# Kernel tuning notes

Measured on AMD Instinct MI355X. Metric: run time of the kernel, lower is better.

The kernel has to match this reference:

```python
import jax, jax.numpy as jnp
import numpy as np

B, S, E, H = 2, 2048, 1024, 16
D = E // H  # head_dim = 64


def setup_inputs() -> dict:
    key = jax.random.key(0)
    ks = jax.random.split(key, 8)
    s = 0.02
    return {
        "queries": jax.random.normal(ks[0], (B, S, E), jnp.float32),
        "keys": jax.random.normal(ks[1], (B, S, E), jnp.float32),
        "values": jax.random.normal(ks[2], (B, S, E), jnp.float32),
        "mask": jnp.ones((B, 1, 1, S), jnp.int32),
        "Wq": jax.random.normal(ks[3], (E, E), jnp.float32) * s,
        "bq": jnp.zeros((E,), jnp.float32),
        "Wk": jax.random.normal(ks[4], (E, E), jnp.float32) * s,
        "bk": jnp.zeros((E,), jnp.float32),
        "Wv": jax.random.normal(ks[5], (E, E), jnp.float32) * s,
        "bv": jnp.zeros((E,), jnp.float32),
        "Wo": jax.random.normal(ks[6], (E, E), jnp.float32) * s,
        "bo": jnp.zeros((E,), jnp.float32),
    }


def reference(queries, keys, values, mask, Wq, bq, Wk, bk, Wv, bv, Wo, bo):
    # NOTE: faithful to source, W_v is applied to the `keys` input; `values` is unused.
    q = queries @ Wq.T + bq            # [B,S,E]
    k = keys @ Wk.T + bk               # [B,S,E]
    v = keys @ Wv.T + bv               # [B,S,E]
    q = q.reshape(B, S, H, D)
    k = k.reshape(B, S, H, D)
    v = v.reshape(B, S, H, D)
    scale = 1.0 / jnp.sqrt(jnp.asarray(D, q.dtype))
    scores = jnp.einsum("nqhd,nkhd->nhqk", q, k)   # [B,H,S,S] full score matrix
    scores = jnp.where(mask == 0, jnp.asarray(-1e20, scores.dtype), scores)
    attn = jax.nn.softmax(scores * scale, axis=-1)
    out = jnp.einsum("nhqk,nkhd->nqhd", attn, v).reshape(B, S, E)
    return out @ Wo.T + bo
```

## Files before the change

kernel.cpp:

```cpp
#include <hip/hip_runtime.h>
#include <hip/hip_bf16.h>
#include <stdint.h>

#define NB 2
#define NS 2048
#define NE 1024
#define NH 16
#define ND 64
#define NT 32

typedef __attribute__((ext_vector_type(4))) float f32x4;
typedef __attribute__((ext_vector_type(16))) float f32x16;
typedef __attribute__((ext_vector_type(8))) short s16x8;
typedef __attribute__((ext_vector_type(4))) unsigned short u16x4;
typedef __attribute__((ext_vector_type(2))) unsigned int uint2v;

__device__ __forceinline__ unsigned short f2bf(float f) {
  union { float f; unsigned int i; } u; u.f = f;
  unsigned int r = u.i + 0x7FFFu + ((u.i >> 16) & 1u);
  return (unsigned short)(r >> 16);
}

__device__ __forceinline__ unsigned cvtpk_bf16(float lo, float hi) {
  unsigned r;
  asm("v_cvt_pk_bf16_f32 %0, %1, %2" : "=v"(r) : "v"(lo), "v"(hi));
  return r;
}

__device__ __forceinline__ void gload_lds16(const void* g, void* l) {
  __builtin_amdgcn_global_load_lds(
      (const __attribute__((address_space(1))) uint32_t*)g,
      (__attribute__((address_space(3))) uint32_t*)l, 16, 0, 0);
}

__device__ __forceinline__ f32x4 mfma16(s16x8 a, s16x8 b, f32x4 c) {
  return __builtin_amdgcn_mfma_f32_16x16x32_bf16(a, b, c, 0, 0, 0);
}
__device__ __forceinline__ f32x16 mfma32(s16x8 a, s16x8 b, f32x16 c) {
  return __builtin_amdgcn_mfma_f32_32x32x16_bf16(a, b, c, 0, 0, 0);
}

__global__ void conv_x2(const float* __restrict__ a, const float* __restrict__ b,
                        unsigned short* __restrict__ da, unsigned short* __restrict__ db,
                        int n4) {
  const float* s = blockIdx.y ? b : a;
  unsigned short* d = blockIdx.y ? db : da;
  int i = blockIdx.x * blockDim.x + threadIdx.x;
  int stride = gridDim.x * blockDim.x;
  for (; i < n4; i += stride) {
    float4 v = ((const float4*)s)[i];
    u16x4 o;
    o.x = f2bf(v.x); o.y = f2bf(v.y); o.z = f2bf(v.z); o.w = f2bf(v.w);
    ((u16x4*)d)[i] = o;
  }
}

__global__ void conv_w4(const float* __restrict__ s0, const float* __restrict__ s1,
                        const float* __restrict__ s2, const float* __restrict__ s3,
                        unsigned short* __restrict__ d0, unsigned short* __restrict__ d1,
                        unsigned short* __restrict__ d2, unsigned short* __restrict__ d3,
                        int n4) {
  const float* s; unsigned short* d;
  switch (blockIdx.y) {
    case 0: s = s0; d = d0; break;
    case 1: s = s1; d = d1; break;
    case 2: s = s2; d = d2; break;
    default: s = s3; d = d3; break;
  }
  int i = blockIdx.x * blockDim.x + threadIdx.x;
  int stride = gridDim.x * blockDim.x;
  for (; i < n4; i += stride) {
    float4 v = ((const float4*)s)[i];
    u16x4 o;
    o.x = f2bf(v.x); o.y = f2bf(v.y); o.z = f2bf(v.z); o.w = f2bf(v.w);
    ((u16x4*)d)[i] = o;
  }
}

__global__ void mask_pack(const int* __restrict__ mask, unsigned long long* __restrict__ bm) {
  int w = blockIdx.x;
  int lane = threadIdx.x;
  int mk = mask[w * 64 + lane];
  unsigned long long bal = __ballot(mk != 0);
  if (lane == 0) bm[w] = bal;
}

__global__ __launch_bounds__(256, 3) void gemm_qkv(
    const unsigned short* __restrict__ Aq, const unsigned short* __restrict__ Akv,
    const unsigned short* __restrict__ Wqp, const unsigned short* __restrict__ Wkp,
    const unsigned short* __restrict__ Wvp,
    const float* __restrict__ bqp, const float* __restrict__ bkp, const float* __restrict__ bvp,
    unsigned short* __restrict__ outq, unsigned short* __restrict__ outk,
    unsigned short* __restrict__ outvt) {
  constexpr int BM = 64, K = 1024;
  __shared__ char smem[2 * (BM * 128 + 16384)];
  const int t = threadIdx.x;
  const int lane = t & 63;
  const int wv = t >> 6;
  const int wr = wv >> 1, wc = wv & 1;
  const int x = blockIdx.x;
  const int bm = blockIdx.y * BM;
  const int lr = lane & 15, lg = lane >> 4;

  const unsigned short* A; const unsigned short* Wp; const float* bp;
  unsigned short* outp; int nloc, mode;
  float qsc;
  if (x < 8)       { A = Aq;  Wp = Wqp; bp = bqp; outp = outq;  nloc = x * 128;        mode = 0; qsc = 0.18033688f; }
  else if (x < 16) { A = Akv; Wp = Wkp; bp = bkp; outp = outk;  nloc = (x - 8) * 128;  mode = 0; qsc = 1.0f; }
  else             { A = Akv; Wp = Wvp; bp = bvp; outp = outvt; nloc = (x - 16) * 128; mode = 1; qsc = 1.0f; }

  f32x4 acc[2][4] = {};

  auto stage = [&](int buf, int k0) {
    char* As = smem + buf * (BM * 128 + 16384);
    char* Bs = As + BM * 128;
#pragma unroll
    for (int r = 0; r < 2; ++r) {
      int lin = r * 256 + t;
      int row = lin >> 3;
      int scb = ((lin & 7) << 4) ^ ((row & 7) << 4);
      gload_lds16((const char*)(A + (size_t)(bm + row) * K + k0) + scb,
                  As + (size_t)(r * 256 + (t & ~63)) * 16);
    }
#pragma unroll
    for (int r = 0; r < 4; ++r) {
      int lin = r * 256 + t;
      int row = lin >> 3;
      int scb = ((lin & 7) << 4) ^ ((row & 7) << 4);
      gload_lds16((const char*)(Wp + (size_t)(nloc + row) * K + k0) + scb,
                  Bs + (size_t)(r * 256 + (t & ~63)) * 16);
    }
  };

  stage(0, 0);
  for (int t6 = 0; t6 < K / 64; ++t6) {
    const int cur = t6 & 1;
    if (t6 + 1 < K / 64) {
      stage(cur ^ 1, (t6 + 1) * 64);
      asm volatile("s_waitcnt vmcnt(6)" ::: "memory");
    } else {
      asm volatile("s_waitcnt vmcnt(0)" ::: "memory");
    }
    asm volatile("s_barrier" ::: "memory");

    const char* As = smem + cur * (BM * 128 + 16384);
    const char* Bs = As + BM * 128;
    s16x8 af[2][2], bfr[4][2];
#pragma unroll
    for (int mf = 0; mf < 2; ++mf)
#pragma unroll
      for (int kk = 0; kk < 2; ++kk) {
        int row = wr * 32 + mf * 16 + lr;
        int cb = (lg << 4) + (kk << 6);
        af[mf][kk] = *(const s16x8*)(As + row * 128 + (cb ^ ((row & 7) << 4)));
      }
#pragma unroll
    for (int nf = 0; nf < 4; ++nf)
#pragma unroll
      for (int kk = 0; kk < 2; ++kk) {
        int row = wc * 64 + nf * 16 + lr;
        int cb = (lg << 4) + (kk << 6);
        bfr[nf][kk] = *(const s16x8*)(Bs + row * 128 + (cb ^ ((row & 7) << 4)));
      }
#pragma unroll
    for (int mf = 0; mf < 2; ++mf)
#pragma unroll
      for (int nf = 0; nf < 4; ++nf)
#pragma unroll
        for (int kk = 0; kk < 2; ++kk)
          acc[mf][nf] = mfma16(af[mf][kk], bfr[nf][kk], acc[mf][nf]);

    asm volatile("s_waitcnt lgkmcnt(0)" ::: "memory");
    asm volatile("s_barrier" ::: "memory");
  }

#pragma unroll
  for (int mf = 0; mf < 2; ++mf)
#pragma unroll
    for (int nf = 0; nf < 4; ++nf) {
      int m0 = bm + wr * 32 + mf * 16 + (lg << 2);
      int nc = wc * 64 + nf * 16 + lr;
      float bv = bp[nloc + nc];
      if (mode == 0) {
#pragma unroll
        for (int r = 0; r < 4; ++r)
          outp[(size_t)(m0 + r) * 1024 + nloc + nc] = f2bf((acc[mf][nf][r] + bv) * qsc);
      } else {
        int b = m0 >> 11, s = m0 & 2047;
        u16x4 o;
        o.x = f2bf(acc[mf][nf][0] + bv);
        o.y = f2bf(acc[mf][nf][1] + bv);
        o.z = f2bf(acc[mf][nf][2] + bv);
        o.w = f2bf(acc[mf][nf][3] + bv);
        *(u16x4*)&outp[((size_t)b * NE + nloc + nc) * NS + s] = o;
      }
    }
}

__global__ __launch_bounds__(256, 3) void gemm_o(
    const unsigned short* __restrict__ A, const unsigned short* __restrict__ W,
    const float* __restrict__ bias, float* __restrict__ out) {
  constexpr int BM = 64, K = 1024;
  __shared__ char smem[2 * (BM * 128 + 16384)];
  const int t = threadIdx.x;
  const int lane = t & 63;
  const int wv = t >> 6;
  const int wr = wv >> 1, wc = wv & 1;
  const int bm = blockIdx.y * BM, bn = blockIdx.x * 128;
  const int lr = lane & 15, lg = lane >> 4;

  f32x4 acc[2][4] = {};

  auto stage = [&](int buf, int k0) {
    char* As = smem + buf * (BM * 128 + 16384);
    char* Bs = As + BM * 128;
#pragma unroll
    for (int r = 0; r < 2; ++r) {
      int lin = r * 256 + t;
      int row = lin >> 3;
      int scb = ((lin & 7) << 4) ^ ((row & 7) << 4);
      gload_lds16((const char*)(A + (size_t)(bm + row) * K + k0) + scb,
                  As + (size_t)(r * 256 + (t & ~63)) * 16);
    }
#pragma unroll
    for (int r = 0; r < 4; ++r) {
      int lin = r * 256 + t;
      int row = lin >> 3;
      int scb = ((lin & 7) << 4) ^ ((row & 7) << 4);
      gload_lds16((const char*)(W + (size_t)(bn + row) * K + k0) + scb,
                  Bs + (size_t)(r * 256 + (t & ~63)) * 16);
    }
  };

  stage(0, 0);
  for (int t6 = 0; t6 < K / 64; ++t6) {
    const int cur = t6 & 1;
    if (t6 + 1 < K / 64) {
      stage(cur ^ 1, (t6 + 1) * 64);
      asm volatile("s_waitcnt vmcnt(6)" ::: "memory");
    } else {
      asm volatile("s_waitcnt vmcnt(0)" ::: "memory");
    }
    asm volatile("s_barrier" ::: "memory");

    const char* As = smem + cur * (BM * 128 + 16384);
    const char* Bs = As + BM * 128;
    s16x8 af[2][2], bfr[4][2];
#pragma unroll
    for (int mf = 0; mf < 2; ++mf)
#pragma unroll
      for (int kk = 0; kk < 2; ++kk) {
        int row = wr * 32 + mf * 16 + lr;
        int cb = (lg << 4) + (kk << 6);
        af[mf][kk] = *(const s16x8*)(As + row * 128 + (cb ^ ((row & 7) << 4)));
      }
#pragma unroll
    for (int nf = 0; nf < 4; ++nf)
#pragma unroll
      for (int kk = 0; kk < 2; ++kk) {
        int row = wc * 64 + nf * 16 + lr;
        int cb = (lg << 4) + (kk << 6);
        bfr[nf][kk] = *(const s16x8*)(Bs + row * 128 + (cb ^ ((row & 7) << 4)));
      }
#pragma unroll
    for (int mf = 0; mf < 2; ++mf)
#pragma unroll
      for (int nf = 0; nf < 4; ++nf)
#pragma unroll
        for (int kk = 0; kk < 2; ++kk)
          acc[mf][nf] = mfma16(af[mf][kk], bfr[nf][kk], acc[mf][nf]);

    asm volatile("s_waitcnt lgkmcnt(0)" ::: "memory");
    asm volatile("s_barrier" ::: "memory");
  }

#pragma unroll
  for (int mf = 0; mf < 2; ++mf)
#pragma unroll
    for (int nf = 0; nf < 4; ++nf) {
      int m0 = bm + wr * 32 + mf * 16 + (lg << 2);
      int n = bn + wc * 64 + nf * 16 + lr;
      float bv = bias[n];
#pragma unroll
      for (int r = 0; r < 4; ++r)
        out[(size_t)(m0 + r) * 1024 + n] = acc[mf][nf][r] + bv;
    }
}

__global__ __launch_bounds__(256, 2) void attn_fwd(
    const unsigned short* __restrict__ qb, const unsigned short* __restrict__ kb,
    const unsigned short* __restrict__ vt, const unsigned long long* __restrict__ bmw,
    unsigned short* __restrict__ ob) {
  __shared__ char smem[65536];
  const int t = threadIdx.x, lane = t & 63, wv = t >> 6;
  const int l31 = lane & 31, hi = lane >> 5;
  const int sw = (l31 & 15) << 4;
  const int bh = blockIdx.y, b = bh >> 4, h = bh & 15;
  const int q = blockIdx.x * 128 + wv * 32 + l31;

  s16x8 qf[4];
#pragma unroll
  for (int ks = 0; ks < 4; ++ks)
    qf[ks] = *(const s16x8*)&qb[((size_t)(b * NS + q)) * NE + h * ND + ks * 16 + hi * 8];

  unsigned long long mword = bmw[(size_t)b * 32 + l31];
  unsigned mlo = (unsigned)mword, mhi = (unsigned)(mword >> 32);

  const char* kSrc[2]; const char* vSrc[2]; int ldsK[2], ldsV[2];
#pragma unroll
  for (int r = 0; r < 2; ++r) {
    int L = (r * 256 + t) * 16;
    int row = L >> 8;
    int offp = (L & 255) ^ ((row & 15) << 4);
    int rr = row + ((offp >> 7) << 5);
    int byo = offp & 127;
    kSrc[r] = (const char*)&kb[((size_t)(b * NS) + rr) * NE + h * ND] + byo;
    vSrc[r] = (const char*)&vt[((size_t)((b * NH + h) * ND) + rr) * NS] + byo;
    ldsK[r] = (r * 256 + (t & ~63)) * 16;
    ldsV[r] = 8192 + ldsK[r];
  }

  int off16[8];
#pragma unroll
  for (int j = 0; j < 8; ++j)
    off16[j] = l31 * 256 + ((j * 32 + hi * 16) ^ sw);

  auto stage = [&](int buf, int kt) {
    char* base = smem + buf * 16384;
#pragma unroll
    for (int r = 0; r < 2; ++r)
      gload_lds16(kSrc[r] + (size_t)kt * (NE * 2), base + ldsK[r]);
#pragma unroll
    for (int r = 0; r < 2; ++r)
      gload_lds16(vSrc[r] + (size_t)kt * 2, base + ldsV[r]);
  };

  f32x16 oacc[2] = {};
  f32x16 lacc = {};

  auto compute = [&](int tt, const char* Ks) {
    const char* Vs = Ks + 8192;

    f32x16 st0 = {}, st1 = {};
    __builtin_amdgcn_s_setprio(1);
#pragma unroll
    for (int ks = 0; ks < 4; ++ks) {
      s16x8 kf = *(const s16x8*)(Ks + off16[ks]);
      st0 = mfma32(kf, qf[ks], st0);
    }
#pragma unroll
    for (int ks = 0; ks < 4; ++ks) {
      s16x8 kf = *(const s16x8*)(Ks + off16[4 + ks]);
      st1 = mfma32(kf, qf[ks], st1);
    }
    __builtin_amdgcn_s_setprio(0);

#pragma unroll
    for (int r = 0; r < 16; ++r) st0[r] = __builtin_amdgcn_exp2f(st0[r] - 6.0f);
#pragma unroll
    for (int r = 0; r < 16; ++r) st1[r] = __builtin_amdgcn_exp2f(st1[r] - 6.0f);

    unsigned lo = (unsigned)__builtin_amdgcn_readlane((int)mlo, tt);
    unsigned hh = (unsigned)__builtin_amdgcn_readlane((int)mhi, tt);
    unsigned long long bal = ((unsigned long long)hh << 32) | lo;
    if (bal != ~0ull) {
#pragma unroll
      for (int r = 0; r < 16; ++r) {
        int key0 = (r & 3) + 8 * (r >> 2) + 4 * hi;
        if (!((bal >> key0) & 1)) st0[r] = 0.f;
        if (!((bal >> (key0 + 32)) & 1)) st1[r] = 0.f;
      }
    }

    lacc += st0;
    lacc += st1;

    s16x8 pf[4];
#pragma unroll
    for (int ks = 0; ks < 4; ++ks) {
      const int r0 = (ks & 1) * 8;
      unsigned wreg[4];
#pragma unroll
      for (int w = 0; w < 2; ++w) {
        float e0, e1, e2, e3;
        if (ks < 2) {
          e0 = st0[r0 + 2 * w]; e1 = st0[r0 + 2 * w + 1];
          e2 = st0[r0 + 4 + 2 * w]; e3 = st0[r0 + 4 + 2 * w + 1];
        } else {
          e0 = st1[r0 + 2 * w]; e1 = st1[r0 + 2 * w + 1];
          e2 = st1[r0 + 4 + 2 * w]; e3 = st1[r0 + 4 + 2 * w + 1];
        }
        unsigned x = cvtpk_bf16(e0, e1);
        unsigned y = cvtpk_bf16(e2, e3);
        uint2v r2 = __builtin_amdgcn_permlane32_swap(x, y, false, false);
        wreg[w] = r2.x;
        wreg[w + 2] = r2.y;
      }
      union { unsigned u[4]; s16x8 v; } pu;
      pu.u[0] = wreg[0]; pu.u[1] = wreg[1]; pu.u[2] = wreg[2]; pu.u[3] = wreg[3];
      pf[ks] = pu.v;
    }

    __builtin_amdgcn_s_setprio(1);
#pragma unroll
    for (int td = 0; td < 2; ++td)
#pragma unroll
      for (int ks = 0; ks < 4; ++ks) {
        s16x8 vf = *(const s16x8*)(Vs + off16[td * 4 + ks]);
        oacc[td] = mfma32(vf, pf[ks], oacc[td]);
      }
    __builtin_amdgcn_s_setprio(0);
  };

  stage(0, 0);
  stage(1, 64);

#pragma unroll 1
  for (int tt = 0; tt < NT; tt += 4) {
    asm volatile("s_waitcnt vmcnt(0)" ::: "memory");
    __builtin_amdgcn_s_barrier();
    if (tt + 2 < NT) { stage(2, (tt + 2) * 64); stage(3, (tt + 3) * 64); }
    compute(tt + 0, smem);
    compute(tt + 1, smem + 16384);
    asm volatile("s_waitcnt vmcnt(0)" ::: "memory");
    __builtin_amdgcn_s_barrier();
    if (tt + 4 < NT) { stage(0, (tt + 4) * 64); stage(1, (tt + 5) * 64); }
    compute(tt + 2, smem + 32768);
    compute(tt + 3, smem + 49152);
  }

  float l0 = 0.f;
#pragma unroll
  for (int r = 0; r < 16; ++r) l0 += lacc[r];
  float l = l0 + __shfl_xor(l0, 32);
  float inv = 1.0f / l;

  char* Ob = smem + wv * 4096;
#pragma unroll
  for (int td = 0; td < 2; ++td)
#pragma unroll
    for (int i = 0; i < 8; ++i) {
      int r = 2 * i;
      int d = td * 32 + (r & 3) + 8 * (r >> 2) + 4 * hi;
      unsigned pk = cvtpk_bf16(oacc[td][r] * inv, oacc[td][r + 1] * inv);
      *(unsigned*)(Ob + l31 * 128 + ((d * 2) ^ ((l31 & 7) << 4))) = pk;
    }
#pragma unroll
  for (int p4 = 0; p4 < 4; ++p4) {
    int lq = p4 * 8 + (lane >> 3);
    int col = (lane & 7) * 16;
    s16x8 v0 = *(const s16x8*)(Ob + lq * 128 + (col ^ ((lq & 7) << 4)));
    int qg = blockIdx.x * 128 + wv * 32 + lq;
    *(s16x8*)((char*)&ob[((size_t)(b * NS + qg)) * NE + h * ND] + col) = v0;
  }
}

extern "C" void kernel_launch(void* const* d_in, const int* in_sizes, int n_in,
                              void* d_out, int out_size, void* d_ws, size_t ws_size,
                              hipStream_t stream) {
  const float* queries = (const float*)d_in[0];
  const float* keys = (const float*)d_in[1];
  const int* mask = (const int*)d_in[3];
  const float* Wq = (const float*)d_in[4];
  const float* bq = (const float*)d_in[5];
  const float* Wk = (const float*)d_in[6];
  const float* bk = (const float*)d_in[7];
  const float* Wv = (const float*)d_in[8];
  const float* bv = (const float*)d_in[9];
  const float* Wo = (const float*)d_in[10];
  const float* bo = (const float*)d_in[11];
  float* out = (float*)d_out;

  char* ws = (char*)d_ws;
  const size_t SZ_X = (size_t)NB * NS * NE * 2;
  const size_t SZ_W = (size_t)NE * NE * 2;
  unsigned short* qbf = (unsigned short*)(ws);
  unsigned short* kbf = (unsigned short*)(ws + SZ_X);
  unsigned short* wqb = (unsigned short*)(ws + 2 * SZ_X);
  unsigned short* wkb = (unsigned short*)(ws + 2 * SZ_X + SZ_W);
  unsigned short* wvb = (unsigned short*)(ws + 2 * SZ_X + 2 * SZ_W);
  unsigned short* wob = (unsigned short*)(ws + 2 * SZ_X + 3 * SZ_W);
  unsigned short* qp  = (unsigned short*)(ws + 2 * SZ_X + 4 * SZ_W);
  unsigned short* kp  = (unsigned short*)(ws + 3 * SZ_X + 4 * SZ_W);
  unsigned short* vtp = (unsigned short*)(ws + 4 * SZ_X + 4 * SZ_W);
  unsigned short* ao  = (unsigned short*)(ws + 5 * SZ_X + 4 * SZ_W);
  unsigned long long* bmp = (unsigned long long*)(ws + 6 * SZ_X + 4 * SZ_W);

  int nX4 = NB * NS * NE / 4, nW4 = NE * NE / 4;
  conv_x2<<<dim3(1024, 2), 256, 0, stream>>>(queries, keys, qbf, kbf, nX4);
  conv_w4<<<dim3(256, 4), 256, 0, stream>>>(Wq, Wk, Wv, Wo, wqb, wkb, wvb, wob, nW4);
  mask_pack<<<NB * NS / 64, 64, 0, stream>>>(mask, bmp);

  gemm_qkv<<<dim3(24, 64), 256, 0, stream>>>(qbf, kbf, wqb, wkb, wvb,
                                             bq, bk, bv, qp, kp, vtp);

  dim3 ga(NS / 128, NB * NH);
  attn_fwd<<<ga, 256, 0, stream>>>(qp, kp, vtp, bmp, ao);

  gemm_o<<<dim3(8, 64), 256, 0, stream>>>(ao, wob, bo, out);
}
```

Before: 119.6 us.

## Software-pipeline QK of next tile with PV of previous tile in attention loop

Restructures the attention inner loop so that each iteration issues the QK^T MFMAs for tile t together with the PV MFMAs for tile t-1, with softmax/pack of tile t happening afterwards. This lets matrix work overlap the exp/pack VALU work instead of running them back to back. The staging also changes from two tiles per barrier with vmcnt(0) to a 4-slot ring with one tile staged per iteration and a partial vmcnt(4) wait, giving finer-grained prefetch. It costs an extra barrier per tile and keeps the packed P fragments live across iterations, which raises register pressure.

```diff
diff --git a/kernel.cpp b/kernel.cpp
--- a/kernel.cpp
+++ b/kernel.cpp
@@ -337,12 +337,9 @@
 
   f32x16 oacc[2] = {};
   f32x16 lacc = {};
-
-  auto compute = [&](int tt, const char* Ks) {
-    const char* Vs = Ks + 8192;
-
-    f32x16 st0 = {}, st1 = {};
-    __builtin_amdgcn_s_setprio(1);
+  s16x8 pfp[4];
+
+  auto qk = [&](const char* Ks, f32x16& st0, f32x16& st1) {
 #pragma unroll
     for (int ks = 0; ks < 4; ++ks) {
       s16x8 kf = *(const s16x8*)(Ks + off16[ks]);
@@ -353,8 +350,19 @@
       s16x8 kf = *(const s16x8*)(Ks + off16[4 + ks]);
       st1 = mfma32(kf, qf[ks], st1);
     }
-    __builtin_amdgcn_s_setprio(0);
-
+  };
+
+  auto pv = [&](const char* Vs) {
+#pragma unroll
+    for (int td = 0; td < 2; ++td)
+#pragma unroll
+      for (int ks = 0; ks < 4; ++ks) {
+        s16x8 vf = *(const s16x8*)(Vs + off16[td * 4 + ks]);
+        oacc[td] = mfma32(vf, pfp[ks], oacc[td]);
+      }
+  };
+
+  auto smpack = [&](int tt, f32x16& st0, f32x16& st1) {
 #pragma unroll
     for (int r = 0; r < 16; ++r) st0[r] = __builtin_amdgcn_exp2f(st0[r] - 6.0f);
 #pragma unroll
@@ -375,7 +383,6 @@
     lacc += st0;
     lacc += st1;
 
-    s16x8 pf[4];
 #pragma unroll
     for (int ks = 0; ks < 4; ++ks) {
       const int r0 = (ks & 1) * 8;
@@ -398,36 +405,47 @@
       }
       union { unsigned u[4]; s16x8 v; } pu;
       pu.u[0] = wreg[0]; pu.u[1] = wreg[1]; pu.u[2] = wreg[2]; pu.u[3] = wreg[3];
-      pf[ks] = pu.v;
-    }
-
-    __builtin_amdgcn_s_setprio(1);
-#pragma unroll
-    for (int td = 0; td < 2; ++td)
-#pragma unroll
-      for (int ks = 0; ks < 4; ++ks) {
-        s16x8 vf = *(const s16x8*)(Vs + off16[td * 4 + ks]);
-        oacc[td] = mfma32(vf, pf[ks], oacc[td]);
-      }
-    __builtin_amdgcn_s_setprio(0);
+      pfp[ks] = pu.v;
+    }
   };
 
   stage(0, 0);
   stage(1, 64);
 
+  asm volatile("s_waitcnt vmcnt(4)" ::: "memory");
+  __builtin_amdgcn_s_barrier();
+  stage(2, 128);
+  {
+    f32x16 s0 = {}, s1 = {};
+    __builtin_amdgcn_s_setprio(1);
+    qk(smem, s0, s1);
+    __builtin_amdgcn_s_setprio(0);
+    smpack(0, s0, s1);
+  }
+
 #pragma unroll 1
-  for (int tt = 0; tt < NT; tt += 4) {
-    asm volatile("s_waitcnt vmcnt(0)" ::: "memory");
+  for (int tt = 1; tt < NT; ++tt) {
+    if (tt + 1 < NT) {
+      asm volatile("s_waitcnt vmcnt(4)" ::: "memory");
+    } else {
+      asm volatile("s_waitcnt vmcnt(0)" ::: "memory");
+    }
     __builtin_amdgcn_s_barrier();
-    if (tt + 2 < NT) { stage(2, (tt + 2) * 64); stage(3, (tt + 3) * 64); }
-    compute(tt + 0, smem);
-    compute(tt + 1, smem + 16384);
-    asm volatile("s_waitcnt vmcnt(0)" ::: "memory");
-    __builtin_amdgcn_s_barrier();
-    if (tt + 4 < NT) { stage(0, (tt + 4) * 64); stage(1, (tt + 5) * 64); }
-    compute(tt + 2, smem + 32768);
-    compute(tt + 3, smem + 49152);
-  }
+    if (tt + 2 < NT) stage((tt + 2) & 3, (tt + 2) * 64);
+
+    const char* Kb = smem + (tt & 3) * 16384;
+    const char* Vb = smem + ((tt - 1) & 3) * 16384 + 8192;
+    f32x16 s0 = {}, s1 = {};
+    __builtin_amdgcn_s_setprio(1);
+    qk(Kb, s0, s1);
+    pv(Vb);
+    __builtin_amdgcn_s_setprio(0);
+    smpack(tt, s0, s1);
+  }
+
+  __builtin_amdgcn_s_setprio(1);
+  pv(smem + ((NT - 1) & 3) * 16384 + 8192);
+  __builtin_amdgcn_s_setprio(0);
 
   float l0 = 0.f;
 #pragma unroll
```

Measured after the change: 115.7 us. 1.03x faster.
